# Kernel tuning notes

Measured on AMD Instinct MI355X. Metric: run time of the kernel, lower is better.

Reference implementation:

```python
import jax, jax.numpy as jnp
import numpy as np

B, N, K = 2, 131072, 9
P, D, S, CI, CO = 4, 4, 1, 8, 8
NH_DIST = 1.0
MIN_SIGMA = 1e-10


def setup_inputs() -> dict:
    key = jax.random.key(0)
    ks = jax.random.split(key, 6)
    x = jax.random.normal(ks[0], (B, N, CI), dtype=jnp.float32)
    # relative cartesian coordinates of each neighbor w.r.t. reference node
    dx = jax.random.normal(ks[1], (B, N, K), dtype=jnp.float32) * 0.5
    dy = jax.random.normal(ks[2], (B, N, K), dtype=jnp.float32) * 0.5
    adj = jax.random.randint(ks[3], (N, K), 0, N, dtype=jnp.int32)
    # fixed polar kernel centers as in __init__
    phis = jnp.linspace(-jnp.pi, jnp.pi, P + 1)[:-1].astype(jnp.float32)
    dists = jnp.linspace(0.0, NH_DIST, D + 2)[1:-1].astype(jnp.float32)
    sigma = jnp.cumsum(jnp.diff(dists))[:S].astype(jnp.float32)
    # amplitudes_no: (n_phi, n_dist, n_sigma, n_amps_in, n_amps_out), xavier-like
    scale = np.sqrt(6.0 / (CI + CO))
    amplitudes_no = jax.random.uniform(ks[4], (P, D, S, CI, CO), dtype=jnp.float32,
                                       minval=-scale, maxval=scale)
    return {"x": x, "dx": dx, "dy": dy, "adj": adj,
            "phis": phis, "dists": dists, "sigma": sigma,
            "amplitudes_no": amplitudes_no}


def reference(x, dx, dy, adj, phis, dists, sigma, amplitudes_no):
    # irregular neighbor gather (get_nh): [B, N, K, CI]
    x_nh = x[:, adj]
    # polar Gaussian kernel centers in cartesian: [P, D]
    mus_lon = jnp.cos(phis)[:, None] * dists[None, :]
    mus_lat = jnp.sin(phis)[:, None] * dists[None, :]
    # offsets: [B, N, K, P, D]
    ddx = dx[..., None, None] - mus_lon
    ddy = dy[..., None, None] - mus_lat
    sig = jnp.clip(sigma, MIN_SIGMA)  # [S]
    r2 = ddx * ddx + ddy * ddy  # [B, N, K, P, D]
    # Gaussian basis weights: [B, N, K, P, D, S]
    w = jnp.exp(-0.5 * r2[..., None] / (sig * sig)) / jnp.sqrt(2.0 * jnp.pi * sig * sig)
    # gather-compute-aggregate: sum over neighbors k and input amplitudes c
    out = jnp.einsum('bnkpds,bnkc,pdsco->bnpdso', w, x_nh, amplitudes_no)
    return out
```

## Files before the change

### kernel.cpp

```cpp
#include <hip/hip_runtime.h>
#include <math.h>

#define N_PTS 131072
#define KNB   9
#define PD    16
#define CIN   8
#define COUT  8
#define PTS_PER_BLK 16
#define THREADS 256
#define AMP_STRIDE 68

__global__ __launch_bounds__(THREADS) void polnormal_kernel(
    const float* __restrict__ x,
    const float* __restrict__ dx,
    const float* __restrict__ dy,
    const int*   __restrict__ adj,
    const float* __restrict__ phis,
    const float* __restrict__ dists,
    const float* __restrict__ sigma,
    const float* __restrict__ amp,
    float*       __restrict__ out)
{
    __shared__ float s_dx[PTS_PER_BLK * KNB];
    __shared__ float s_dy[PTS_PER_BLK * KNB];
    __shared__ int   s_adj[PTS_PER_BLK * KNB];
    __shared__ float s_x[PTS_PER_BLK * KNB * CIN];
    __shared__ float s_amp[PD * AMP_STRIDE];

    const int  tid    = threadIdx.x;
    const long base_g = (long)blockIdx.x * PTS_PER_BLK;
    const int  b      = (int)(base_g >> 17);
    const int  base_n = (int)(base_g & (N_PTS - 1));

    if (tid < PTS_PER_BLK * KNB) {
        s_dx[tid]  = dx[base_g * KNB + tid];
        s_dy[tid]  = dy[base_g * KNB + tid];
        s_adj[tid] = adj[(long)base_n * KNB + tid];
    }
    for (int t = tid; t < PD * CIN * COUT; t += THREADS) {
        int pd = t >> 6;
        int co = t & 63;
        s_amp[pd * AMP_STRIDE + co] = amp[t];
    }
    __syncthreads();

    for (int t = tid; t < PTS_PER_BLK * KNB * 2; t += THREADS) {
        int pair = t >> 1;
        int half = t & 1;
        long row = (long)s_adj[pair];
        const float4* src = (const float4*)(x + ((long)b * N_PTS + row) * CIN);
        ((float4*)s_x)[pair * 2 + half] = src[half];
    }
    __syncthreads();

    const int i  = tid >> 4;
    const int pd = tid & 15;
    const int p  = pd >> 2;
    const int d  = pd & 3;

    const float phi  = phis[p];
    const float dist = dists[d];
    float sn, cs;
    __sincosf(phi, &sn, &cs);
    const float mux = cs * dist;
    const float muy = sn * dist;

    float sig = fmaxf(sigma[0], 1e-10f);
    const float s2         = sig * sig;
    const float neg_inv2s2 = -0.5f / s2;
    const float norm       = rsqrtf(6.283185307179586f * s2);

    float wx[CIN];
#pragma unroll
    for (int c = 0; c < CIN; ++c) wx[c] = 0.0f;

#pragma unroll
    for (int k = 0; k < KNB; ++k) {
        float ddx = s_dx[i * KNB + k] - mux;
        float ddy = s_dy[i * KNB + k] - muy;
        float r2  = ddx * ddx + ddy * ddy;
        float w   = __expf(neg_inv2s2 * r2) * norm;
        const float* xr = &s_x[(i * KNB + k) * CIN];
#pragma unroll
        for (int c = 0; c < CIN; ++c) wx[c] += w * xr[c];
    }

    float acc[COUT];
#pragma unroll
    for (int o = 0; o < COUT; ++o) acc[o] = 0.0f;
#pragma unroll
    for (int c = 0; c < CIN; ++c) {
        const float wc = wx[c];
        const float* ar = &s_amp[pd * AMP_STRIDE + c * COUT];
#pragma unroll
        for (int o = 0; o < COUT; ++o) acc[o] += wc * ar[o];
    }

    float4* op = (float4*)(out + ((base_g + i) * PD + pd) * COUT);
    op[0] = make_float4(acc[0], acc[1], acc[2], acc[3]);
    op[1] = make_float4(acc[4], acc[5], acc[6], acc[7]);
}

extern "C" void kernel_launch(void* const* d_in, const int* in_sizes, int n_in,
                              void* d_out, int out_size, void* d_ws, size_t ws_size,
                              hipStream_t stream) {
    const float* x     = (const float*)d_in[0];
    const float* dx    = (const float*)d_in[1];
    const float* dy    = (const float*)d_in[2];
    const int*   adj   = (const int*)  d_in[3];
    const float* phis  = (const float*)d_in[4];
    const float* dists = (const float*)d_in[5];
    const float* sigma = (const float*)d_in[6];
    const float* amp   = (const float*)d_in[7];
    float* out = (float*)d_out;

    const int total_pts = 2 * N_PTS;
    const int grid = total_pts / PTS_PER_BLK;
    polnormal_kernel<<<grid, THREADS, 0, stream>>>(x, dx, dy, adj, phis, dists,
                                                   sigma, amp, out);
}
```

Baseline: 207.9 us.

## Process four points per thread with 64-point blocks and vectorized nontemporal IO

Each block now handles 64 points, and each thread computes four points for its (p,d) pair. This amortizes the per-block amplitude table load and the per-thread setup (sincos, sigma) over more work, and reuses the amplitude vectors across points. Loads of dx, dy and adj are vectorized with nontemporal hints, and outputs use nontemporal float4 stores to cut cache pollution on the streaming traffic. The costs are higher register use and fewer blocks, which can lower occupancy and latency hiding for the gather of x.

```diff
diff --git a/kernel.cpp b/kernel.cpp
--- a/kernel.cpp
+++ b/kernel.cpp
@@ -6,9 +6,13 @@
 #define PD    16
 #define CIN   8
 #define COUT  8
-#define PTS_PER_BLK 16
+#define PTS_PER_BLK 64
+#define PTS_PER_THREAD 4
 #define THREADS 256
 #define AMP_STRIDE 68
+
+typedef float vf4 __attribute__((ext_vector_type(4)));
+typedef int   vi4 __attribute__((ext_vector_type(4)));
 
 __global__ __launch_bounds__(THREADS) void polnormal_kernel(
     const float* __restrict__ x,
@@ -32,10 +36,13 @@
     const int  b      = (int)(base_g >> 17);
     const int  base_n = (int)(base_g & (N_PTS - 1));
 
-    if (tid < PTS_PER_BLK * KNB) {
-        s_dx[tid]  = dx[base_g * KNB + tid];
-        s_dy[tid]  = dy[base_g * KNB + tid];
-        s_adj[tid] = adj[(long)base_n * KNB + tid];
+    if (tid < (PTS_PER_BLK * KNB) / 4) {
+        const vf4* pdx = (const vf4*)(dx + base_g * KNB);
+        const vf4* pdy = (const vf4*)(dy + base_g * KNB);
+        const vi4* pad = (const vi4*)(adj + (long)base_n * KNB);
+        ((vf4*)s_dx)[tid] = __builtin_nontemporal_load(pdx + tid);
+        ((vf4*)s_dy)[tid] = __builtin_nontemporal_load(pdy + tid);
+        ((vi4*)s_adj)[tid] = __builtin_nontemporal_load(pad + tid);
     }
     for (int t = tid; t < PD * CIN * COUT; t += THREADS) {
         int pd = t >> 6;
@@ -44,16 +51,17 @@
     }
     __syncthreads();
 
-    for (int t = tid; t < PTS_PER_BLK * KNB * 2; t += THREADS) {
-        int pair = t >> 1;
-        int half = t & 1;
-        long row = (long)s_adj[pair];
-        const float4* src = (const float4*)(x + ((long)b * N_PTS + row) * CIN);
-        ((float4*)s_x)[pair * 2 + half] = src[half];
+    {
+        const vf4* xb = (const vf4*)x + (long)b * N_PTS * 2;
+        for (int t = tid; t < PTS_PER_BLK * KNB * 2; t += THREADS) {
+            int pair = t >> 1;
+            int half = t & 1;
+            ((vf4*)s_x)[t] = xb[(long)s_adj[pair] * 2 + half];
+        }
     }
     __syncthreads();
 
-    const int i  = tid >> 4;
+    const int i0 = tid >> 4;
     const int pd = tid & 15;
     const int p  = pd >> 2;
     const int d  = pd & 3;
@@ -65,40 +73,65 @@
     const float mux = cs * dist;
     const float muy = sn * dist;
 
-    float sig = fmaxf(sigma[0], 1e-10f);
+    const float sig        = fmaxf(sigma[0], 1e-10f);
     const float s2         = sig * sig;
     const float neg_inv2s2 = -0.5f / s2;
     const float norm       = rsqrtf(6.283185307179586f * s2);
 
-    float wx[CIN];
+    float wx[PTS_PER_THREAD][CIN];
 #pragma unroll
-    for (int c = 0; c < CIN; ++c) wx[c] = 0.0f;
+    for (int j = 0; j < PTS_PER_THREAD; ++j)
+#pragma unroll
+        for (int c = 0; c < CIN; ++c) wx[j][c] = 0.0f;
 
 #pragma unroll
     for (int k = 0; k < KNB; ++k) {
-        float ddx = s_dx[i * KNB + k] - mux;
-        float ddy = s_dy[i * KNB + k] - muy;
-        float r2  = ddx * ddx + ddy * ddy;
-        float w   = __expf(neg_inv2s2 * r2) * norm;
-        const float* xr = &s_x[(i * KNB + k) * CIN];
 #pragma unroll
-        for (int c = 0; c < CIN; ++c) wx[c] += w * xr[c];
+        for (int j = 0; j < PTS_PER_THREAD; ++j) {
+            const int i   = i0 + 16 * j;
+            const int ik  = i * KNB + k;
+            float ddx = s_dx[ik] - mux;
+            float ddy = s_dy[ik] - muy;
+            float r2  = ddx * ddx + ddy * ddy;
+            float w   = __expf(neg_inv2s2 * r2) * norm;
+            const vf4* xr = (const vf4*)&s_x[ik * CIN];
+            vf4 x0 = xr[0], x1 = xr[1];
+            wx[j][0] += w * x0.x; wx[j][1] += w * x0.y;
+            wx[j][2] += w * x0.z; wx[j][3] += w * x0.w;
+            wx[j][4] += w * x1.x; wx[j][5] += w * x1.y;
+            wx[j][6] += w * x1.z; wx[j][7] += w * x1.w;
+        }
     }
 
-    float acc[COUT];
+    float acc[PTS_PER_THREAD][COUT];
 #pragma unroll
-    for (int o = 0; o < COUT; ++o) acc[o] = 0.0f;
+    for (int j = 0; j < PTS_PER_THREAD; ++j)
+#pragma unroll
+        for (int o = 0; o < COUT; ++o) acc[j][o] = 0.0f;
+
 #pragma unroll
     for (int c = 0; c < CIN; ++c) {
-        const float wc = wx[c];
-        const float* ar = &s_amp[pd * AMP_STRIDE + c * COUT];
+        const vf4* ar = (const vf4*)&s_amp[pd * AMP_STRIDE + c * COUT];
+        vf4 a0 = ar[0], a1 = ar[1];
 #pragma unroll
-        for (int o = 0; o < COUT; ++o) acc[o] += wc * ar[o];
+        for (int j = 0; j < PTS_PER_THREAD; ++j) {
+            const float wc = wx[j][c];
+            acc[j][0] += wc * a0.x; acc[j][1] += wc * a0.y;
+            acc[j][2] += wc * a0.z; acc[j][3] += wc * a0.w;
+            acc[j][4] += wc * a1.x; acc[j][5] += wc * a1.y;
+            acc[j][6] += wc * a1.z; acc[j][7] += wc * a1.w;
+        }
     }
 
-    float4* op = (float4*)(out + ((base_g + i) * PD + pd) * COUT);
-    op[0] = make_float4(acc[0], acc[1], acc[2], acc[3]);
-    op[1] = make_float4(acc[4], acc[5], acc[6], acc[7]);
+#pragma unroll
+    for (int j = 0; j < PTS_PER_THREAD; ++j) {
+        const int i = i0 + 16 * j;
+        vf4* op = (vf4*)(out + ((base_g + i) * PD + pd) * COUT);
+        vf4 lo = {acc[j][0], acc[j][1], acc[j][2], acc[j][3]};
+        vf4 hi = {acc[j][4], acc[j][5], acc[j][6], acc[j][7]};
+        __builtin_nontemporal_store(lo, op);
+        __builtin_nontemporal_store(hi, op + 1);
+    }
 }
 
 extern "C" void kernel_launch(void* const* d_in, const int* in_sizes, int n_in,
```

Result: slower. 257.9 us (+24.0%).

## Gather neighbor features directly from global memory and drop shared staging

Applied to the files above, without the earlier changes.

Removes the shared-memory staging of gathered neighbor features and the second block barrier. Each thread now loads its neighbor rows straight from global memory, so the 16 threads that share a point issue duplicate loads that the cache must absorb. The change also vectorizes the dx/dy/adj loads to 16-byte accesses, uses exp2 with a pre-scaled constant, packs the arithmetic into 2-wide float vectors, and writes the output with nontemporal stores.

```diff
diff --git a/kernel.cpp b/kernel.cpp
--- a/kernel.cpp
+++ b/kernel.cpp
@@ -9,6 +9,10 @@
 #define PTS_PER_BLK 16
 #define THREADS 256
 #define AMP_STRIDE 68
+
+typedef float vf2 __attribute__((ext_vector_type(2)));
+typedef float vf4 __attribute__((ext_vector_type(4)));
+typedef int   vi4 __attribute__((ext_vector_type(4)));
 
 __global__ __launch_bounds__(THREADS) void polnormal_kernel(
     const float* __restrict__ x,
@@ -24,7 +28,6 @@
     __shared__ float s_dx[PTS_PER_BLK * KNB];
     __shared__ float s_dy[PTS_PER_BLK * KNB];
     __shared__ int   s_adj[PTS_PER_BLK * KNB];
-    __shared__ float s_x[PTS_PER_BLK * KNB * CIN];
     __shared__ float s_amp[PD * AMP_STRIDE];
 
     const int  tid    = threadIdx.x;
@@ -32,26 +35,19 @@
     const int  b      = (int)(base_g >> 17);
     const int  base_n = (int)(base_g & (N_PTS - 1));
 
-    if (tid < PTS_PER_BLK * KNB) {
-        s_dx[tid]  = dx[base_g * KNB + tid];
-        s_dy[tid]  = dy[base_g * KNB + tid];
-        s_adj[tid] = adj[(long)base_n * KNB + tid];
+    if (tid < (PTS_PER_BLK * KNB) / 4) {
+        const vf4* pdx = (const vf4*)(dx + base_g * KNB);
+        const vf4* pdy = (const vf4*)(dy + base_g * KNB);
+        const vi4* pad = (const vi4*)(adj + (long)base_n * KNB);
+        ((vf4*)s_dx)[tid]  = pdx[tid];
+        ((vf4*)s_dy)[tid]  = pdy[tid];
+        ((vi4*)s_adj)[tid] = pad[tid];
     }
     for (int t = tid; t < PD * CIN * COUT; t += THREADS) {
-        int pd = t >> 6;
-        int co = t & 63;
-        s_amp[pd * AMP_STRIDE + co] = amp[t];
+        int pdi = t >> 6;
+        int co  = t & 63;
+        s_amp[pdi * AMP_STRIDE + co] = amp[t];
     }
-    __syncthreads();
-
-    for (int t = tid; t < PTS_PER_BLK * KNB * 2; t += THREADS) {
-        int pair = t >> 1;
-        int half = t & 1;
-        long row = (long)s_adj[pair];
-        const float4* src = (const float4*)(x + ((long)b * N_PTS + row) * CIN);
-        ((float4*)s_x)[pair * 2 + half] = src[half];
-    }
-    __syncthreads();
 
     const int i  = tid >> 4;
     const int pd = tid & 15;
@@ -65,40 +61,52 @@
     const float mux = cs * dist;
     const float muy = sn * dist;
 
-    float sig = fmaxf(sigma[0], 1e-10f);
-    const float s2         = sig * sig;
-    const float neg_inv2s2 = -0.5f / s2;
-    const float norm       = rsqrtf(6.283185307179586f * s2);
+    const float sig   = fmaxf(sigma[0], 1e-10f);
+    const float s2    = sig * sig;
+    const float k2    = (-0.5f / s2) * 1.4426950408889634f;
+    const float norm  = rsqrtf(6.283185307179586f * s2);
 
-    float wx[CIN];
-#pragma unroll
-    for (int c = 0; c < CIN; ++c) wx[c] = 0.0f;
+    __syncthreads();
+
+    const vf4* xb = (const vf4*)x + (long)b * N_PTS * 2;
+
+    vf2 wx01 = {0.f, 0.f}, wx23 = {0.f, 0.f}, wx45 = {0.f, 0.f}, wx67 = {0.f, 0.f};
 
 #pragma unroll
     for (int k = 0; k < KNB; ++k) {
-        float ddx = s_dx[i * KNB + k] - mux;
-        float ddy = s_dy[i * KNB + k] - muy;
-        float r2  = ddx * ddx + ddy * ddy;
-        float w   = __expf(neg_inv2s2 * r2) * norm;
-        const float* xr = &s_x[(i * KNB + k) * CIN];
-#pragma unroll
-        for (int c = 0; c < CIN; ++c) wx[c] += w * xr[c];
+        const int ik = i * KNB + k;
+        const long row = (long)s_adj[ik];
+        vf4 x0 = xb[row * 2];
+        vf4 x1 = xb[row * 2 + 1];
+        float ddx = s_dx[ik] - mux;
+        float ddy = s_dy[ik] - muy;
+        float r2  = __builtin_fmaf(ddx, ddx, ddy * ddy);
+        float w   = __builtin_amdgcn_exp2f(k2 * r2) * norm;
+        wx01 += w * x0.xy;
+        wx23 += w * x0.zw;
+        wx45 += w * x1.xy;
+        wx67 += w * x1.zw;
     }
 
-    float acc[COUT];
-#pragma unroll
-    for (int o = 0; o < COUT; ++o) acc[o] = 0.0f;
+    vf2 ac01 = {0.f, 0.f}, ac23 = {0.f, 0.f}, ac45 = {0.f, 0.f}, ac67 = {0.f, 0.f};
+    const float wxs[CIN] = {wx01.x, wx01.y, wx23.x, wx23.y,
+                            wx45.x, wx45.y, wx67.x, wx67.y};
 #pragma unroll
     for (int c = 0; c < CIN; ++c) {
-        const float wc = wx[c];
-        const float* ar = &s_amp[pd * AMP_STRIDE + c * COUT];
-#pragma unroll
-        for (int o = 0; o < COUT; ++o) acc[o] += wc * ar[o];
+        const vf4* ar = (const vf4*)&s_amp[pd * AMP_STRIDE + c * COUT];
+        vf4 a0 = ar[0], a1 = ar[1];
+        const float wc = wxs[c];
+        ac01 += wc * a0.xy;
+        ac23 += wc * a0.zw;
+        ac45 += wc * a1.xy;
+        ac67 += wc * a1.zw;
     }
 
-    float4* op = (float4*)(out + ((base_g + i) * PD + pd) * COUT);
-    op[0] = make_float4(acc[0], acc[1], acc[2], acc[3]);
-    op[1] = make_float4(acc[4], acc[5], acc[6], acc[7]);
+    vf4* op = (vf4*)(out + ((base_g + i) * PD + pd) * COUT);
+    vf4 lo = {ac01.x, ac01.y, ac23.x, ac23.y};
+    vf4 hi = {ac45.x, ac45.y, ac67.x, ac67.y};
+    __builtin_nontemporal_store(lo, op);
+    __builtin_nontemporal_store(hi, op + 1);
 }
 
 extern "C" void kernel_launch(void* const* d_in, const int* in_sizes, int n_in,
```

Measured after the change: 213.1 us. 1.02x slower.

## Assign one point per thread, drop shared memory, use register-resident gathers

Applied to the files above, without the earlier changes.

Changes the work split so each thread handles one point and all 16 polar/dist bins, instead of 16 threads per point sharing staged data in LDS. Neighbour features, dx/dy and adjacency are loaded straight into registers, which removes the shared-memory staging and both block barriers. The amplitude matrix is read from global/scalar memory, exp is replaced by exp2 with a folded constant, and outputs use nontemporal stores. The cost is heavy register pressure per thread and per-thread output writes of 512 bytes that are strided across lanes, so stores coalesce less well.

```diff
diff --git a/kernel.cpp b/kernel.cpp
--- a/kernel.cpp
+++ b/kernel.cpp
@@ -3,14 +3,16 @@
 
 #define N_PTS 131072
 #define KNB   9
-#define PD    16
+#define PDN   16
 #define CIN   8
 #define COUT  8
-#define PTS_PER_BLK 16
-#define THREADS 256
-#define AMP_STRIDE 68
+#define THREADS 64
 
-__global__ __launch_bounds__(THREADS) void polnormal_kernel(
+typedef float vf4  __attribute__((ext_vector_type(4)));
+typedef float vf4u __attribute__((ext_vector_type(4), aligned(4)));
+typedef int   vi4u __attribute__((ext_vector_type(4), aligned(4)));
+
+__global__ __launch_bounds__(THREADS, 4) void polnormal_kernel(
     const float* __restrict__ x,
     const float* __restrict__ dx,
     const float* __restrict__ dy,
@@ -21,84 +23,77 @@
     const float* __restrict__ amp,
     float*       __restrict__ out)
 {
-    __shared__ float s_dx[PTS_PER_BLK * KNB];
-    __shared__ float s_dy[PTS_PER_BLK * KNB];
-    __shared__ int   s_adj[PTS_PER_BLK * KNB];
-    __shared__ float s_x[PTS_PER_BLK * KNB * CIN];
-    __shared__ float s_amp[PD * AMP_STRIDE];
+    const int pt = blockIdx.x * THREADS + threadIdx.x;
+    const int b  = pt >> 17;
+    const int n  = pt & (N_PTS - 1);
 
-    const int  tid    = threadIdx.x;
-    const long base_g = (long)blockIdx.x * PTS_PER_BLK;
-    const int  b      = (int)(base_g >> 17);
-    const int  base_n = (int)(base_g & (N_PTS - 1));
+    const int* ap = adj + (long)n * KNB;
+    vi4u a03 = *(const vi4u*)ap;
+    vi4u a47 = *(const vi4u*)(ap + 4);
+    int  a8  = ap[8];
+    int rows[KNB] = {a03.x, a03.y, a03.z, a03.w, a47.x, a47.y, a47.z, a47.w, a8};
 
-    if (tid < PTS_PER_BLK * KNB) {
-        s_dx[tid]  = dx[base_g * KNB + tid];
-        s_dy[tid]  = dy[base_g * KNB + tid];
-        s_adj[tid] = adj[(long)base_n * KNB + tid];
+    const vf4* xb = (const vf4*)x + (long)b * (N_PTS * 2);
+    vf4 xlo[KNB], xhi[KNB];
+#pragma unroll
+    for (int k = 0; k < KNB; ++k) {
+        long r2i = (long)rows[k] * 2;
+        xlo[k] = xb[r2i];
+        xhi[k] = xb[r2i + 1];
     }
-    for (int t = tid; t < PD * CIN * COUT; t += THREADS) {
-        int pd = t >> 6;
-        int co = t & 63;
-        s_amp[pd * AMP_STRIDE + co] = amp[t];
-    }
-    __syncthreads();
 
-    for (int t = tid; t < PTS_PER_BLK * KNB * 2; t += THREADS) {
-        int pair = t >> 1;
-        int half = t & 1;
-        long row = (long)s_adj[pair];
-        const float4* src = (const float4*)(x + ((long)b * N_PTS + row) * CIN);
-        ((float4*)s_x)[pair * 2 + half] = src[half];
-    }
-    __syncthreads();
+    const float* dxp = dx + (long)pt * KNB;
+    const float* dyp = dy + (long)pt * KNB;
+    vf4u dxa = *(const vf4u*)dxp, dxb2 = *(const vf4u*)(dxp + 4);
+    vf4u dya = *(const vf4u*)dyp, dyb2 = *(const vf4u*)(dyp + 4);
+    float dxv[KNB] = {dxa.x, dxa.y, dxa.z, dxa.w, dxb2.x, dxb2.y, dxb2.z, dxb2.w, dxp[8]};
+    float dyv[KNB] = {dya.x, dya.y, dya.z, dya.w, dyb2.x, dyb2.y, dyb2.z, dyb2.w, dyp[8]};
 
-    const int i  = tid >> 4;
-    const int pd = tid & 15;
-    const int p  = pd >> 2;
-    const int d  = pd & 3;
+    const float sig  = fmaxf(sigma[0], 1e-10f);
+    const float s2   = sig * sig;
+    const float k2   = (-0.5f / s2) * 1.4426950408889634f;
+    const float norm = rsqrtf(6.283185307179586f * s2);
 
-    const float phi  = phis[p];
-    const float dist = dists[d];
-    float sn, cs;
-    __sincosf(phi, &sn, &cs);
-    const float mux = cs * dist;
-    const float muy = sn * dist;
-
-    float sig = fmaxf(sigma[0], 1e-10f);
-    const float s2         = sig * sig;
-    const float neg_inv2s2 = -0.5f / s2;
-    const float norm       = rsqrtf(6.283185307179586f * s2);
-
-    float wx[CIN];
-#pragma unroll
-    for (int c = 0; c < CIN; ++c) wx[c] = 0.0f;
+    float* op = out + (long)pt * (PDN * COUT);
 
 #pragma unroll
-    for (int k = 0; k < KNB; ++k) {
-        float ddx = s_dx[i * KNB + k] - mux;
-        float ddy = s_dy[i * KNB + k] - muy;
-        float r2  = ddx * ddx + ddy * ddy;
-        float w   = __expf(neg_inv2s2 * r2) * norm;
-        const float* xr = &s_x[(i * KNB + k) * CIN];
+    for (int pd = 0; pd < PDN; ++pd) {
+        const int p = pd >> 2, d = pd & 3;
+        float sn, cs;
+        __sincosf(phis[p], &sn, &cs);
+        const float dist = dists[d];
+        const float mux = cs * dist, muy = sn * dist;
+
+        float w[KNB];
 #pragma unroll
-        for (int c = 0; c < CIN; ++c) wx[c] += w * xr[c];
+        for (int k = 0; k < KNB; ++k) {
+            float ddx = dxv[k] - mux;
+            float ddy = dyv[k] - muy;
+            w[k] = __builtin_amdgcn_exp2f(k2 * __builtin_fmaf(ddx, ddx, ddy * ddy));
+        }
+
+        vf4 wxA = {0.f, 0.f, 0.f, 0.f}, wxB = {0.f, 0.f, 0.f, 0.f};
+#pragma unroll
+        for (int k = 0; k < KNB; ++k) {
+            wxA += w[k] * xlo[k];
+            wxB += w[k] * xhi[k];
+        }
+
+        const float wxs[CIN] = {wxA.x, wxA.y, wxA.z, wxA.w,
+                                wxB.x, wxB.y, wxB.z, wxB.w};
+        vf4 accA = {0.f, 0.f, 0.f, 0.f}, accB = {0.f, 0.f, 0.f, 0.f};
+        const float* ar = amp + pd * (CIN * COUT);
+#pragma unroll
+        for (int c = 0; c < CIN; ++c) {
+            vf4 ampA = *(const vf4*)(ar + c * COUT);
+            vf4 ampB = *(const vf4*)(ar + c * COUT + 4);
+            accA += wxs[c] * ampA;
+            accB += wxs[c] * ampB;
+        }
+
+        __builtin_nontemporal_store(accA * norm, (vf4*)(op + pd * COUT));
+        __builtin_nontemporal_store(accB * norm, (vf4*)(op + pd * COUT + 4));
     }
-
-    float acc[COUT];
-#pragma unroll
-    for (int o = 0; o < COUT; ++o) acc[o] = 0.0f;
-#pragma unroll
-    for (int c = 0; c < CIN; ++c) {
-        const float wc = wx[c];
-        const float* ar = &s_amp[pd * AMP_STRIDE + c * COUT];
-#pragma unroll
-        for (int o = 0; o < COUT; ++o) acc[o] += wc * ar[o];
-    }
-
-    float4* op = (float4*)(out + ((base_g + i) * PD + pd) * COUT);
-    op[0] = make_float4(acc[0], acc[1], acc[2], acc[3]);
-    op[1] = make_float4(acc[4], acc[5], acc[6], acc[7]);
 }
 
 extern "C" void kernel_launch(void* const* d_in, const int* in_sizes, int n_in,
@@ -115,7 +110,7 @@
     float* out = (float*)d_out;
 
     const int total_pts = 2 * N_PTS;
-    const int grid = total_pts / PTS_PER_BLK;
+    const int grid = total_pts / THREADS;
     polnormal_kernel<<<grid, THREADS, 0, stream>>>(x, dx, dy, adj, phis, dists,
                                                    sigma, amp, out);
 }
```

Result: slower. 487.0 us (+134.2%).
